# Optimization experiments

Measured on AMD Instinct MI355X. Metric: run time of the kernel, lower is better.

Reference implementation:

```python
import jax, jax.numpy as jnp
import numpy as np

N_NODES = 1_000_000
BATCH = 100_000
DIM_NIG = 128
DIM_NODE = 128


def setup_inputs() -> dict:
    key = jax.random.key(0)
    ks = jax.random.split(key, 9)
    return {
        "src_node_ids": jax.random.randint(ks[0], (BATCH,), 0, N_NODES),
        "dst_node_ids": jax.random.randint(ks[1], (BATCH,), 0, N_NODES),
        "previous_embedding": jax.random.normal(ks[2], (N_NODES, DIM_NODE), jnp.float32),
        "batch_src_neighbor_embedding": jax.random.normal(ks[3], (BATCH, DIM_NIG), jnp.float32),
        "batch_dst_neighbor_embedding": jax.random.normal(ks[4], (BATCH, DIM_NIG), jnp.float32),
        # neighbor_layer: Linear(dim_nig -> dim_node); torch weight layout [out, in]
        "W_nig": jax.random.normal(ks[5], (DIM_NODE, DIM_NIG), jnp.float32) / np.sqrt(DIM_NIG),
        "b_nig": jax.random.normal(ks[6], (DIM_NODE,), jnp.float32) * 0.01,
        # node_layer: Linear(dim_node -> dim_node)
        "W_node": jax.random.normal(ks[7], (DIM_NODE, DIM_NODE), jnp.float32) / np.sqrt(DIM_NODE),
        "b_node": jax.random.normal(ks[8], (DIM_NODE,), jnp.float32) * 0.01,
    }


def _update(prev_emb, node_ids, nbr_emb, W_nig, b_nig, W_node, b_node):
    prev = jnp.take(prev_emb, node_ids, axis=0)          # [B, D] gather
    shift = nbr_emb @ W_nig.T + b_nig                    # [B, D]
    return (prev + shift) @ W_node.T + b_node + prev     # linear + residual


def reference(src_node_ids, dst_node_ids, previous_embedding,
              batch_src_neighbor_embedding, batch_dst_neighbor_embedding,
              W_nig, b_nig, W_node, b_node):
    src_emb = _update(previous_embedding, src_node_ids, batch_src_neighbor_embedding,
                      W_nig, b_nig, W_node, b_node)
    dst_emb = _update(previous_embedding, dst_node_ids, batch_dst_neighbor_embedding,
                      W_nig, b_nig, W_node, b_node)
    # clone().detach() in torch -> stop_gradient base, then scatter src then dst
    updated = jax.lax.stop_gradient(previous_embedding)
    updated = updated.at[src_node_ids].set(src_emb)
    updated = updated.at[dst_node_ids].set(dst_emb)
    return updated
```

## Files before the change

### kernel.cpp

```cpp
#include <hip/hip_runtime.h>
#include <hip/hip_bf16.h>

#define B_SZ 100000
#define NTOT 200000
#define NN   1000000
#define DIM  128

#define NB_INIT   3907
#define NB_WFRAG  32
#define NB_CLAIM  782

#define TILES     62500
#define GRID_MAIN 512
#define BLK_MAIN  512
#define WAVES_TOT (GRID_MAIN * 8)

typedef short bf16x8 __attribute__((ext_vector_type(8)));
typedef float f32x4  __attribute__((ext_vector_type(4)));

__device__ __forceinline__ short f2bf(float f) {
    union { float f; unsigned u; } v; v.f = f;
    unsigned u = v.u;
    u += 0x7fffu + ((u >> 16) & 1u);
    return (short)(u >> 16);
}

__global__ __launch_bounds__(256) void k_init_weights(
        int* __restrict__ owner,
        const float* __restrict__ Wnig, const float* __restrict__ bnig,
        const float* __restrict__ Wnode, const float* __restrict__ bnode,
        short* __restrict__ PA, short* __restrict__ PQ,
        float* __restrict__ cvec) {
    int b = blockIdx.x, t = threadIdx.x;
    if (b < NB_INIT) {
        int i = b * 256 + t;
        if (i < NN) owner[i] = -1;
    } else if (b < NB_INIT + NB_WFRAG) {
        int b2 = b - NB_INIT;
        int lane = t & 63, ig = t >> 6;
        int kc = b2 >> 3, nc = b2 & 7;
        int n = nc * 16 + (lane & 15);
        int kbase = kc * 32 + (lane >> 4) * 8;
        int fo = (b2 * 64 + lane) * 8;
        for (int ii = 0; ii < 2; ++ii) {
            int i = ig * 2 + ii;
            int k = kbase + i;
            float a = Wnode[n * DIM + k] + (k == n ? 1.0f : 0.0f);
            PA[fo + i] = f2bf(a);
            float q = 0.f;
            for (int m = 0; m < DIM; ++m) q += Wnode[n * DIM + m] * Wnig[m * DIM + k];
            PQ[fo + i] = f2bf(q);
        }
    } else {
        if (t < DIM) {
            float c = bnode[t];
            for (int k = 0; k < DIM; ++k) c += bnig[k] * Wnode[t * DIM + k];
            cvec[t] = c;
        }
    }
}

__global__ void k_claim(const int* __restrict__ src, const int* __restrict__ dst,
                        int* __restrict__ owner) {
    int i = blockIdx.x * 256 + threadIdx.x;
    if (i >= NTOT) return;
    int node = (i < B_SZ) ? src[i] : dst[i - B_SZ];
    atomicMax(&owner[node], i);
}

__global__ __launch_bounds__(BLK_MAIN, 4) void k_node(
        const float* __restrict__ prev,
        const float* __restrict__ nsrc, const float* __restrict__ ndst,
        const int* __restrict__ owner,
        const short* __restrict__ PA, const short* __restrict__ PQ,
        const float* __restrict__ cvec,
        float* __restrict__ out) {
    __shared__ __align__(16) short lA[32 * 64 * 8];
    __shared__ __align__(16) short lQ[32 * 64 * 8];
    int tid = threadIdx.x;
    {
        const float4* gA = (const float4*)PA;
        const float4* gQ = (const float4*)PQ;
        float4* sA = (float4*)lA;
        float4* sQ = (float4*)lQ;
        for (int i = tid; i < 2048; i += BLK_MAIN) { sA[i] = gA[i]; sQ[i] = gQ[i]; }
    }
    __syncthreads();

    int wave = tid >> 6, lane = tid & 63;
    int wid = blockIdx.x * 8 + wave;
    int myrow = lane & 15;
    int koff = (lane >> 4) * 8;
    int col0 = lane & 15;
    int rbase = (lane >> 4) * 4;

    float cv[8];
#pragma unroll
    for (int nc = 0; nc < 8; ++nc) cv[nc] = cvec[nc * 16 + col0];

    for (int tile = wid; tile < TILES; tile += WAVES_TOT) {
        int nbase = tile * 16;
        int my_owner = owner[nbase + myrow];
        unsigned mask16 = (unsigned)(__ballot(my_owner >= 0) & 0xFFFFu);

        if (mask16) {
            const float* prow = prev + (size_t)(nbase + myrow) * DIM;
            const float* nrow = prow;
            if (my_owner >= 0) {
                bool is_src = my_owner < B_SZ;
                int bi = is_src ? my_owner : my_owner - B_SZ;
                nrow = (is_src ? nsrc : ndst) + (size_t)bi * DIM;
            }
            f32x4 acc[8];
#pragma unroll
            for (int nc = 0; nc < 8; ++nc) acc[nc] = (f32x4){0.f, 0.f, 0.f, 0.f};

#pragma unroll
            for (int kc = 0; kc < 4; ++kc) {
                int k0 = kc * 32 + koff;
                bf16x8 aP = (bf16x8){0,0,0,0,0,0,0,0};
                bf16x8 aN = (bf16x8){0,0,0,0,0,0,0,0};
                if (my_owner >= 0) {
                    float4 p0 = *(const float4*)(prow + k0);
                    float4 p1 = *(const float4*)(prow + k0 + 4);
                    float4 n0 = *(const float4*)(nrow + k0);
                    float4 n1 = *(const float4*)(nrow + k0 + 4);
                    aP[0]=f2bf(p0.x); aP[1]=f2bf(p0.y); aP[2]=f2bf(p0.z); aP[3]=f2bf(p0.w);
                    aP[4]=f2bf(p1.x); aP[5]=f2bf(p1.y); aP[6]=f2bf(p1.z); aP[7]=f2bf(p1.w);
                    aN[0]=f2bf(n0.x); aN[1]=f2bf(n0.y); aN[2]=f2bf(n0.z); aN[3]=f2bf(n0.w);
                    aN[4]=f2bf(n1.x); aN[5]=f2bf(n1.y); aN[6]=f2bf(n1.z); aN[7]=f2bf(n1.w);
                }
#pragma unroll
                for (int nc = 0; nc < 8; ++nc) {
                    int fo = ((kc * 8 + nc) * 64 + lane) * 8;
                    bf16x8 bA = *(const bf16x8*)(lA + fo);
                    bf16x8 bQ = *(const bf16x8*)(lQ + fo);
                    acc[nc] = __builtin_amdgcn_mfma_f32_16x16x32_bf16(aP, bA, acc[nc], 0, 0, 0);
                    acc[nc] = __builtin_amdgcn_mfma_f32_16x16x32_bf16(aN, bQ, acc[nc], 0, 0, 0);
                }
            }
#pragma unroll
            for (int r = 0; r < 4; ++r) {
                int rt = rbase + r;
                if ((mask16 >> rt) & 1u) {
                    float* orow = out + (size_t)(nbase + rt) * DIM;
#pragma unroll
                    for (int nc = 0; nc < 8; ++nc)
                        orow[nc * 16 + col0] = acc[nc][r] + cv[nc];
                }
            }
        }

        unsigned um = (~mask16) & 0xFFFFu;
        while (um) {
            int r0 = __builtin_ctz(um); um &= um - 1;
            int r1 = -1;
            if (um) { r1 = __builtin_ctz(um); um &= um - 1; }
            int r = (lane < 32) ? r0 : r1;
            if (r >= 0) {
                const float4* s4 = (const float4*)(prev + (size_t)(nbase + r) * DIM);
                float4* d4 = (float4*)(out + (size_t)(nbase + r) * DIM);
                d4[lane & 31] = s4[lane & 31];
            }
        }
    }
}

extern "C" void kernel_launch(void* const* d_in, const int* in_sizes, int n_in,
                              void* d_out, int out_size, void* d_ws, size_t ws_size,
                              hipStream_t stream) {
    const int*   src  = (const int*)d_in[0];
    const int*   dst  = (const int*)d_in[1];
    const float* prev = (const float*)d_in[2];
    const float* nsrc = (const float*)d_in[3];
    const float* ndst = (const float*)d_in[4];
    const float* Wnig = (const float*)d_in[5];
    const float* bnig = (const float*)d_in[6];
    const float* Wnode = (const float*)d_in[7];
    const float* bnode = (const float*)d_in[8];
    float* out = (float*)d_out;

    const size_t OWNER_B = (size_t)NN * 4;
    const size_t PA_B = 32 * 64 * 8 * 2;
    if (ws_size < OWNER_B + 2 * PA_B + 512) return;
    char* ws = (char*)d_ws;
    int*   owner = (int*)ws;
    short* PA = (short*)(ws + OWNER_B);
    short* PQ = (short*)(ws + OWNER_B + PA_B);
    float* cvec = (float*)(ws + OWNER_B + 2 * PA_B);

    k_init_weights<<<NB_INIT + NB_WFRAG + 1, 256, 0, stream>>>(
        owner, Wnig, bnig, Wnode, bnode, PA, PQ, cvec);
    k_claim<<<NB_CLAIM, 256, 0, stream>>>(src, dst, owner);
    k_node<<<GRID_MAIN, BLK_MAIN, 0, stream>>>(
        prev, nsrc, ndst, owner, PA, PQ, cvec, out);
}
```

Before: 252.7 us.

## Merge claim into prep kernel, memset owner, and unify row loads with prefetch

```diff
diff --git a/kernel.cpp b/kernel.cpp
--- a/kernel.cpp
+++ b/kernel.cpp
@@ -6,9 +6,9 @@
 #define NN   1000000
 #define DIM  128
 
-#define NB_INIT   3907
+#define NB_CLAIM  782
 #define NB_WFRAG  32
-#define NB_CLAIM  782
+#define NB_PREP   (NB_CLAIM + NB_WFRAG + 1)
 
 #define TILES     62500
 #define GRID_MAIN 512
@@ -25,18 +25,29 @@
     return (short)(u >> 16);
 }
 
-__global__ __launch_bounds__(256) void k_init_weights(
+__device__ __forceinline__ bf16x8 cvt8(float4 a, float4 b) {
+    bf16x8 r;
+    r[0]=f2bf(a.x); r[1]=f2bf(a.y); r[2]=f2bf(a.z); r[3]=f2bf(a.w);
+    r[4]=f2bf(b.x); r[5]=f2bf(b.y); r[6]=f2bf(b.z); r[7]=f2bf(b.w);
+    return r;
+}
+
+__global__ __launch_bounds__(256) void k_prep(
+        const int* __restrict__ src, const int* __restrict__ dst,
         int* __restrict__ owner,
         const float* __restrict__ Wnig, const float* __restrict__ bnig,
         const float* __restrict__ Wnode, const float* __restrict__ bnode,
         short* __restrict__ PA, short* __restrict__ PQ,
         float* __restrict__ cvec) {
     int b = blockIdx.x, t = threadIdx.x;
-    if (b < NB_INIT) {
+    if (b < NB_CLAIM) {
         int i = b * 256 + t;
-        if (i < NN) owner[i] = -1;
-    } else if (b < NB_INIT + NB_WFRAG) {
-        int b2 = b - NB_INIT;
+        if (i < NTOT) {
+            int node = (i < B_SZ) ? src[i] : dst[i - B_SZ];
+            atomicMax(&owner[node], i);
+        }
+    } else if (b < NB_CLAIM + NB_WFRAG) {
+        int b2 = b - NB_CLAIM;
         int lane = t & 63, ig = t >> 6;
         int kc = b2 >> 3, nc = b2 & 7;
         int n = nc * 16 + (lane & 15);
@@ -58,14 +69,6 @@
             cvec[t] = c;
         }
     }
-}
-
-__global__ void k_claim(const int* __restrict__ src, const int* __restrict__ dst,
-                        int* __restrict__ owner) {
-    int i = blockIdx.x * 256 + threadIdx.x;
-    if (i >= NTOT) return;
-    int node = (i < B_SZ) ? src[i] : dst[i - B_SZ];
-    atomicMax(&owner[node], i);
 }
 
 __global__ __launch_bounds__(BLK_MAIN, 4) void k_node(
@@ -90,46 +93,63 @@
     int wave = tid >> 6, lane = tid & 63;
     int wid = blockIdx.x * 8 + wave;
     int myrow = lane & 15;
-    int koff = (lane >> 4) * 8;
-    int col0 = lane & 15;
+    int koff  = (lane >> 4) * 8;
+    int col0  = lane & 15;
     int rbase = (lane >> 4) * 4;
 
     float cv[8];
 #pragma unroll
     for (int nc = 0; nc < 8; ++nc) cv[nc] = cvec[nc * 16 + col0];
 
-    for (int tile = wid; tile < TILES; tile += WAVES_TOT) {
-        int nbase = tile * 16;
-        int my_owner = owner[nbase + myrow];
-        unsigned mask16 = (unsigned)(__ballot(my_owner >= 0) & 0xFFFFu);
+    int t = wid;
+    if (t >= TILES) return;
+    int o_cur = owner[t * 16 + myrow];
+
+    for (; t < TILES; t += WAVES_TOT) {
+        int tn = t + WAVES_TOT;
+        int o_nxt = (tn < TILES) ? owner[tn * 16 + myrow] : -1;
+
+        int nbase = t * 16;
+        const float* prow = prev + (size_t)(nbase + myrow) * DIM + koff;
+        float4 pc[8];
+#pragma unroll
+        for (int kc = 0; kc < 4; ++kc) {
+            pc[2*kc]   = *(const float4*)(prow + kc * 32);
+            pc[2*kc+1] = *(const float4*)(prow + kc * 32 + 4);
+        }
+        bool touched = o_cur >= 0;
+        float4 nb[8];
+#pragma unroll
+        for (int i = 0; i < 8; ++i) nb[i] = (float4){0.f, 0.f, 0.f, 0.f};
+        if (touched) {
+            bool is_src = o_cur < B_SZ;
+            int bi = is_src ? o_cur : o_cur - B_SZ;
+            const float* nrow = (is_src ? nsrc : ndst) + (size_t)bi * DIM + koff;
+#pragma unroll
+            for (int kc = 0; kc < 4; ++kc) {
+                nb[2*kc]   = *(const float4*)(nrow + kc * 32);
+                nb[2*kc+1] = *(const float4*)(nrow + kc * 32 + 4);
+            }
+        }
+        unsigned mask16 = (unsigned)__ballot(touched) & 0xFFFFu;
+
+        if (!touched) {
+            float* orow = out + (size_t)(nbase + myrow) * DIM + koff;
+#pragma unroll
+            for (int kc = 0; kc < 4; ++kc) {
+                *(float4*)(orow + kc * 32)     = pc[2*kc];
+                *(float4*)(orow + kc * 32 + 4) = pc[2*kc+1];
+            }
+        }
 
         if (mask16) {
-            const float* prow = prev + (size_t)(nbase + myrow) * DIM;
-            const float* nrow = prow;
-            if (my_owner >= 0) {
-                bool is_src = my_owner < B_SZ;
-                int bi = is_src ? my_owner : my_owner - B_SZ;
-                nrow = (is_src ? nsrc : ndst) + (size_t)bi * DIM;
-            }
             f32x4 acc[8];
 #pragma unroll
             for (int nc = 0; nc < 8; ++nc) acc[nc] = (f32x4){0.f, 0.f, 0.f, 0.f};
-
 #pragma unroll
             for (int kc = 0; kc < 4; ++kc) {
-                int k0 = kc * 32 + koff;
-                bf16x8 aP = (bf16x8){0,0,0,0,0,0,0,0};
-                bf16x8 aN = (bf16x8){0,0,0,0,0,0,0,0};
-                if (my_owner >= 0) {
-                    float4 p0 = *(const float4*)(prow + k0);
-                    float4 p1 = *(const float4*)(prow + k0 + 4);
-                    float4 n0 = *(const float4*)(nrow + k0);
-                    float4 n1 = *(const float4*)(nrow + k0 + 4);
-                    aP[0]=f2bf(p0.x); aP[1]=f2bf(p0.y); aP[2]=f2bf(p0.z); aP[3]=f2bf(p0.w);
-                    aP[4]=f2bf(p1.x); aP[5]=f2bf(p1.y); aP[6]=f2bf(p1.z); aP[7]=f2bf(p1.w);
-                    aN[0]=f2bf(n0.x); aN[1]=f2bf(n0.y); aN[2]=f2bf(n0.z); aN[3]=f2bf(n0.w);
-                    aN[4]=f2bf(n1.x); aN[5]=f2bf(n1.y); aN[6]=f2bf(n1.z); aN[7]=f2bf(n1.w);
-                }
+                bf16x8 aP = cvt8(pc[2*kc], pc[2*kc+1]);
+                bf16x8 aN = cvt8(nb[2*kc], nb[2*kc+1]);
 #pragma unroll
                 for (int nc = 0; nc < 8; ++nc) {
                     int fo = ((kc * 8 + nc) * 64 + lane) * 8;
@@ -150,19 +170,7 @@
                 }
             }
         }
-
-        unsigned um = (~mask16) & 0xFFFFu;
-        while (um) {
-            int r0 = __builtin_ctz(um); um &= um - 1;
-            int r1 = -1;
-            if (um) { r1 = __builtin_ctz(um); um &= um - 1; }
-            int r = (lane < 32) ? r0 : r1;
-            if (r >= 0) {
-                const float4* s4 = (const float4*)(prev + (size_t)(nbase + r) * DIM);
-                float4* d4 = (float4*)(out + (size_t)(nbase + r) * DIM);
-                d4[lane & 31] = s4[lane & 31];
-            }
-        }
+        o_cur = o_nxt;
     }
 }
 
@@ -189,9 +197,9 @@
     short* PQ = (short*)(ws + OWNER_B + PA_B);
     float* cvec = (float*)(ws + OWNER_B + 2 * PA_B);
 
-    k_init_weights<<<NB_INIT + NB_WFRAG + 1, 256, 0, stream>>>(
-        owner, Wnig, bnig, Wnode, bnode, PA, PQ, cvec);
-    k_claim<<<NB_CLAIM, 256, 0, stream>>>(src, dst, owner);
+    hipMemsetAsync(owner, 0xFF, OWNER_B, stream);
+    k_prep<<<NB_PREP, 256, 0, stream>>>(
+        src, dst, owner, Wnig, bnig, Wnode, bnode, PA, PQ, cvec);
     k_node<<<GRID_MAIN, BLK_MAIN, 0, stream>>>(
         prev, nsrc, ndst, owner, PA, PQ, cvec, out);
 }
```

Measured after the change: 261.1 us. +3.3%, slower.
